# Optimization experiments

Measured on AMD Instinct MI355X. Metric: run time of the kernel, lower is better.

Reference implementation:

```python
import jax, jax.numpy as jnp
import numpy as np

DEPTH, DIM, HEADS, DH, MLP, N, B = 6, 192, 12, 16, 768, 256, 32
INNER = HEADS * DH  # 192


def setup_inputs() -> dict:
    key = jax.random.key(0)
    ks = jax.random.split(key, 10)
    w = lambda i, shape: jax.random.normal(ks[i], shape, dtype=jnp.float32) * 0.02
    return {
        'x': jax.random.normal(ks[0], (B, N, DIM), dtype=jnp.float32),
        'ln1_g': jnp.ones((DEPTH, DIM), jnp.float32),
        'ln1_b': jnp.zeros((DEPTH, DIM), jnp.float32),
        'Wq': w(1, (DEPTH, DIM, INNER)),
        'Wkv': w(2, (DEPTH, DIM, 2 * INNER)),
        'lsa_scale': jnp.full((DEPTH, HEADS), DH ** -0.5, dtype=jnp.float32),
        'mix_pre': jax.random.normal(ks[3], (DEPTH, HEADS, HEADS), dtype=jnp.float32),
        'mix_post': jax.random.normal(ks[4], (DEPTH, HEADS, HEADS), dtype=jnp.float32),
        'Wo': w(5, (DEPTH, INNER, DIM)),
        'bo': jnp.zeros((DEPTH, DIM), jnp.float32),
        'ls1': jnp.full((DEPTH, DIM), 0.1, dtype=jnp.float32),
        'ln2_g': jnp.ones((DEPTH, DIM), jnp.float32),
        'ln2_b': jnp.zeros((DEPTH, DIM), jnp.float32),
        'W1': w(6, (DEPTH, DIM, MLP)),
        'b1': jnp.zeros((DEPTH, MLP), jnp.float32),
        'W2': w(7, (DEPTH, MLP, DIM)),
        'b2': jnp.zeros((DEPTH, DIM), jnp.float32),
        'ls2': jnp.full((DEPTH, DIM), 0.1, dtype=jnp.float32),
    }


def _ln(x, g, b, eps=1e-5):
    m = x.mean(-1, keepdims=True)
    v = ((x - m) ** 2).mean(-1, keepdims=True)
    return (x - m) * jax.lax.rsqrt(v + eps) * g + b


def _heads(t, b, n):
    # (b, n, h*d) -> (b, h, n, d)
    return t.reshape(b, n, HEADS, DH).transpose(0, 2, 1, 3)


def _forward(x, ln1_g, ln1_b, Wq, Wkv, lsa_scale, mix_pre, mix_post, Wo, bo,
             ls1, ln2_g, ln2_b, W1, b1, W2, b2, ls2):
    b, n, _ = x.shape
    diag = jnp.arange(n)
    for l in range(DEPTH):
        # --- PreNorm + talking-heads LSA attention + LayerScale(0.1) ---
        h = _ln(x, ln1_g[l], ln1_b[l])
        q = _heads(h @ Wq[l], b, n)
        k, v = jnp.split(h @ Wkv[l], 2, axis=-1)
        k, v = _heads(k, b, n), _heads(v, b, n)
        dots = jnp.einsum('bhid,bhjd->bhij', q, k) * lsa_scale[l][None, :, None, None]
        # LSA: source sets diagonal to -1e-09 (literal, near-zero) when if_patch_attn
        dots = dots.at[:, :, diag, diag].set(-1e-9)
        dots = jnp.einsum('bhij,hg->bgij', dots, mix_pre[l])
        a = jax.nn.softmax(dots, axis=-1)
        a = jnp.einsum('bhij,hg->bgij', a, mix_post[l])
        o = jnp.einsum('bhij,bhjd->bhid', a, v)
        o = o.transpose(0, 2, 1, 3).reshape(b, n, INNER) @ Wo[l] + bo[l]
        x = x + o * ls1[l]
        # --- PreNorm + GELU FFN + LayerScale(0.1) ---
        h2 = _ln(x, ln2_g[l], ln2_b[l])
        f = jax.nn.gelu(h2 @ W1[l] + b1[l], approximate=False) @ W2[l] + b2[l]
        x = x + f * ls2[l]
    return x


def reference(x, ln1_g, ln1_b, Wq, Wkv, lsa_scale, mix_pre, mix_post, Wo, bo,
              ls1, ln2_g, ln2_b, W1, b1, W2, b2, ls2):
    return _forward(x, ln1_g, ln1_b, Wq, Wkv, lsa_scale, mix_pre, mix_post, Wo,
                    bo, ls1, ln2_g, ln2_b, W1, b1, W2, b2, ls2)
```

## Files before the change

kernel.cpp:

```cpp
#include <hip/hip_runtime.h>
#include <hip/hip_bf16.h>

#define DEPTH   6
#define DIM     192
#define HEADS   12
#define DH      16
#define MLPD    768
#define SEQ     256
#define BATCH   32
#define ROWS    (BATCH*SEQ)

typedef __attribute__((ext_vector_type(8))) short short8;
typedef __attribute__((ext_vector_type(4))) float f32x4;
typedef __attribute__((ext_vector_type(4))) _Float16 half4;
typedef __attribute__((ext_vector_type(8))) _Float16 half8;
typedef __hip_bfloat16 bf16_t;
typedef _Float16 f16_t;

__device__ __forceinline__ bf16_t f2b(float v){ return __float2bfloat16(v); }
__device__ __forceinline__ ushort f2u(float v){
    union{ bf16_t b; ushort u; } w; w.b = __float2bfloat16(v); return w.u;
}
__device__ __forceinline__ f16_t u2h(ushort u){ union{ ushort u; f16_t h; } w; w.u = u; return w.h; }
__device__ __forceinline__ ushort h2u(f16_t h){ union{ ushort u; f16_t h; } w; w.h = h; return w.u; }

__device__ __forceinline__ void async16(ushort* lds, const ushort* gp){
    __builtin_amdgcn_global_load_lds(
        (const __attribute__((address_space(1))) uint*)gp,
        (__attribute__((address_space(3))) uint*)lds, 16, 0, 0);
}

__global__ void copy_kernel(const float* __restrict__ x, float* __restrict__ xr, int n){
    int i = blockIdx.x*256 + threadIdx.x;
    if (i < n) xr[i] = x[i];
}

__device__ __forceinline__ void wt_tile(const float* __restrict__ W,
        ushort* __restrict__ WT, int K, int N, int l, int tx, int ty,
        int tid, ushort* T){
    const float* src = W + ((size_t)l*K + tx*64)*N + ty*64;
    ushort* dst = WT + ((size_t)l*N + ty*64)*K + tx*64;
    int r = tid >> 2, c4 = (tid & 3)*16;
    #pragma unroll
    for (int u=0; u<4; u++){
        float4 v = *(const float4*)(src + (size_t)r*N + c4 + u*4);
        T[(c4+u*4+0)*72 + r] = f2u(v.x);
        T[(c4+u*4+1)*72 + r] = f2u(v.y);
        T[(c4+u*4+2)*72 + r] = f2u(v.z);
        T[(c4+u*4+3)*72 + r] = f2u(v.w);
    }
    __syncthreads();
    int n = tid >> 2, k8 = (tid & 3)*16;
    #pragma unroll
    for (int u=0; u<2; u++)
        *(uint4*)(dst + (size_t)n*K + k8 + u*8) = *(uint4*)&T[n*72 + k8 + u*8];
}

__global__ __launch_bounds__(256) void wt_all(
        const float* __restrict__ Wq, const float* __restrict__ Wkv,
        const float* __restrict__ Wo, const float* __restrict__ W1,
        const float* __restrict__ W2,
        ushort* __restrict__ WqT, ushort* __restrict__ WkvT,
        ushort* __restrict__ WoT, ushort* __restrict__ W1T,
        ushort* __restrict__ W2T){
    __shared__ ushort T[64*72];
    int id = blockIdx.x, l = blockIdx.y, tid = threadIdx.x;
    if (id < 9)       wt_tile(Wq,  WqT,  192, 192, l, id/3,       id%3,       tid, T);
    else if (id < 27) wt_tile(Wkv, WkvT, 192, 384, l, (id-9)/6,   (id-9)%6,   tid, T);
    else if (id < 36) wt_tile(Wo,  WoT,  192, 192, l, (id-27)/3,  (id-27)%3,  tid, T);
    else if (id < 72) wt_tile(W1,  W1T,  192, 768, l, (id-36)/12, (id-36)%12, tid, T);
    else              wt_tile(W2,  W2T,  768, 192, l, (id-72)/3,  (id-72)%3,  tid, T);
}

__global__ __launch_bounds__(256) void ln_kernel(
        const float* __restrict__ xres, const float* __restrict__ ln_g,
        const float* __restrict__ ln_b, ushort* __restrict__ out){
    int lane = threadIdx.x & 63, w = threadIdx.x >> 6;
    int row = blockIdx.x*4 + w;
    const float* xr = xres + (size_t)row*DIM;
    float v0 = xr[lane], v1 = xr[lane+64], v2 = xr[lane+128];
    float s = v0+v1+v2;
    #pragma unroll
    for (int off=32; off; off>>=1) s += __shfl_xor(s, off, 64);
    float m = s*(1.0f/192.0f);
    float d0=v0-m, d1=v1-m, d2=v2-m;
    float q = d0*d0+d1*d1+d2*d2;
    #pragma unroll
    for (int off=32; off; off>>=1) q += __shfl_xor(q, off, 64);
    float inv = rsqrtf(q*(1.0f/192.0f) + 1e-5f);
    float g0 = ln_g[lane], g1 = ln_g[lane+64], g2 = ln_g[lane+128];
    float e0 = ln_b[lane], e1 = ln_b[lane+64], e2 = ln_b[lane+128];
    ushort* dst = out + (size_t)row*DIM;
    dst[lane]     = f2u(d0*inv*g0 + e0);
    dst[lane+64]  = f2u(d1*inv*g1 + e1);
    dst[lane+128] = f2u(d2*inv*g2 + e2);
}

template<int MODE>
__global__ __launch_bounds__(256) void gemm_ln_kernel(
        const ushort* __restrict__ Aln, const ushort* __restrict__ BT0,
        const ushort* __restrict__ BT1, const float* __restrict__ bias,
        f16_t* __restrict__ out0, f16_t* __restrict__ out1,
        f16_t* __restrict__ out2){
    __shared__ ushort As[6*2048];
    __shared__ ushort Bs[6*2048];
    int tid = threadIdx.x, lane = tid & 63, w = tid >> 6;
    int bm = blockIdx.x*64;
    int bn = blockIdx.y*64;
    {
        const ushort* ap = Aln + (size_t)(bm + (tid>>2))*DIM + (tid&3)*8;
        const ushort* bt; int bnl;
        if (MODE == 0 && bn >= DIM){ bt = BT1; bnl = bn - DIM; }
        else { bt = BT0; bnl = bn; }
        const ushort* bp = bt + (size_t)(bnl + (tid>>2))*DIM + (tid&3)*8;
        #pragma unroll
        for (int c=0; c<6; c++){
            async16(&As[c*2048 + tid*8], ap + c*32);
            async16(&Bs[c*2048 + tid*8], bp + c*32);
        }
    }
    __syncthreads();
    int wrow = w >> 1, wcol = w & 1;
    int quad = lane >> 4, mr = lane & 15;
    f32x4 acc[2][2] = {};
    #pragma unroll
    for (int c = 0; c < 6; c++){
        short8 a0 = *(const short8*)&As[c*2048 + (wrow*32+mr)*32    + quad*8];
        short8 a1 = *(const short8*)&As[c*2048 + (wrow*32+16+mr)*32 + quad*8];
        short8 b0 = *(const short8*)&Bs[c*2048 + (wcol*32+mr)*32    + quad*8];
        short8 b1 = *(const short8*)&Bs[c*2048 + (wcol*32+16+mr)*32 + quad*8];
        acc[0][0] = __builtin_amdgcn_mfma_f32_16x16x32_bf16(a0, b0, acc[0][0], 0,0,0);
        acc[0][1] = __builtin_amdgcn_mfma_f32_16x16x32_bf16(a0, b1, acc[0][1], 0,0,0);
        acc[1][0] = __builtin_amdgcn_mfma_f32_16x16x32_bf16(a1, b0, acc[1][0], 0,0,0);
        acc[1][1] = __builtin_amdgcn_mfma_f32_16x16x32_bf16(a1, b1, acc[1][1], 0,0,0);
    }
    #pragma unroll
    for (int rr=0; rr<2; rr++){
        #pragma unroll
        for (int cc=0; cc<2; cc++){
            int col = bn + wcol*32 + cc*16 + mr;
            if (MODE == 0){
                if (col < 2*DIM){
                    f16_t* op = (col < DIM) ? (out0 + col) : (out1 + col - DIM);
                    #pragma unroll
                    for (int tt=0; tt<4; tt++){
                        int row = bm + wrow*32 + rr*16 + quad*4 + tt;
                        op[(size_t)row*DIM] = (f16_t)acc[rr][cc][tt];
                    }
                } else {
                    int d = col - 2*DIM;
                    int row0 = bm + wrow*32 + rr*16 + quad*4;
                    int bb = row0 >> 8, j0 = row0 & 255;
                    half4 pk;
                    #pragma unroll
                    for (int tt=0; tt<4; tt++) pk[tt] = (f16_t)acc[rr][cc][tt];
                    *(half4*)(out2 + (((size_t)(bb*DIM + d)) << 8) + j0) = pk;
                }
            } else {
                float bv = bias[col];
                #pragma unroll
                for (int tt=0; tt<4; tt++){
                    int row = bm + wrow*32 + rr*16 + quad*4 + tt;
                    float z = acc[rr][cc][tt] + bv;
                    ((bf16_t*)out0)[(size_t)row*MLPD + col] =
                        f2b(0.5f*z*(1.0f + erff(z*0.70710678118654752f)));
                }
            }
        }
    }
}

template<int ROUNDS>
__global__ __launch_bounds__(256) void gemm_a_kernel(
        const ushort* __restrict__ A, const ushort* __restrict__ BT,
        const float* __restrict__ bias, const float* __restrict__ ls,
        float* __restrict__ xres){
    const int K = ROUNDS*192;
    __shared__ ushort As[6*2048];
    __shared__ ushort Bs[6*2048];
    int tid = threadIdx.x, lane = tid & 63, w = tid >> 6;
    int wrow = w >> 1, wcol = w & 1;
    int bm = blockIdx.x*64, bn = blockIdx.y*64;
    int quad = lane >> 4, mr = lane & 15;
    const ushort* ap = A  + (size_t)(bm + (tid>>2))*K + (tid&3)*8;
    const ushort* bp = BT + (size_t)(bn + (tid>>2))*K + (tid&3)*8;
    f32x4 acc[2][2] = {};
    for (int r = 0; r < ROUNDS; r++){
        #pragma unroll
        for (int c=0; c<6; c++){
            async16(&As[c*2048 + tid*8], ap + r*192 + c*32);
            async16(&Bs[c*2048 + tid*8], bp + r*192 + c*32);
        }
        __syncthreads();
        #pragma unroll
        for (int c=0; c<6; c++){
            short8 a0 = *(const short8*)&As[c*2048 + (wrow*32+mr)*32    + quad*8];
            short8 a1 = *(const short8*)&As[c*2048 + (wrow*32+16+mr)*32 + quad*8];
            short8 b0 = *(const short8*)&Bs[c*2048 + (wcol*32+mr)*32    + quad*8];
            short8 b1 = *(const short8*)&Bs[c*2048 + (wcol*32+16+mr)*32 + quad*8];
            acc[0][0] = __builtin_amdgcn_mfma_f32_16x16x32_bf16(a0, b0, acc[0][0], 0,0,0);
            acc[0][1] = __builtin_amdgcn_mfma_f32_16x16x32_bf16(a0, b1, acc[0][1], 0,0,0);
            acc[1][0] = __builtin_amdgcn_mfma_f32_16x16x32_bf16(a1, b0, acc[1][0], 0,0,0);
            acc[1][1] = __builtin_amdgcn_mfma_f32_16x16x32_bf16(a1, b1, acc[1][1], 0,0,0);
        }
        if (r+1 < ROUNDS) __syncthreads();
    }
    #pragma unroll
    for (int rr=0; rr<2; rr++){
        #pragma unroll
        for (int cc=0; cc<2; cc++){
            int col = bn + wcol*32 + cc*16 + mr;
            float bv = bias[col], lv = ls[col];
            #pragma unroll
            for (int tt=0; tt<4; tt++){
                int row = bm + wrow*32 + rr*16 + quad*4 + tt;
                xres[(size_t)row*DIM + col] += (acc[rr][cc][tt] + bv)*lv;
            }
        }
    }
}

#define SLAB     4488
#define IST      280
#define ROWP     200
#define Q_OFF    53856
#define POST_OFF 57056
#define PRE_OFF  57312
#define X_OFF    57456
#define LTOT     63856

__global__ __launch_bounds__(1024, 1) void attn_kernel(
        const f16_t* __restrict__ qb, const f16_t* __restrict__ kb,
        const f16_t* __restrict__ vTg,
        const float* __restrict__ lsa, const float* __restrict__ pre,
        const float* __restrict__ post, const ushort* __restrict__ WoT,
        const float* __restrict__ bo, const float* __restrict__ ls1,
        const float* __restrict__ ln2g, const float* __restrict__ ln2b,
        ushort* __restrict__ lnb, float* __restrict__ xres){
    __shared__ ushort L[LTOT];
    int tid  = threadIdx.x;
    int lane = tid & 63, w = tid >> 6;
    int quad = lane >> 4, nr = lane & 15;
    int b  = blockIdx.x >> 4;
    int i0 = (blockIdx.x & 15) << 4;

    if (tid < 384){
        int e = tid*8, i = e/DIM, d = e%DIM, hh = d >> 4;
        float sc = lsa[hh];
        union { uint4 v; f16_t h[8]; } iv, ov;
        iv.v = *(const uint4*)(qb + (size_t)(b*SEQ + i0 + i)*DIM + d);
        #pragma unroll
        for (int u=0; u<8; u++) ov.h[u] = (f16_t)((float)iv.h[u]*sc);
        *(uint4*)&L[Q_OFF + i*ROWP + d] = ov.v;
    } else if (tid < 512){
        for (int k = tid-384; k < 256; k += 128){
            int gg = k >> 4, hh = k & 15;
            L[POST_OFF + k] = (gg < 12 && hh < 12) ? h2u((f16_t)post[hh*12+gg])
                                                   : (ushort)0;
        }
    } else if (tid < 640){
        for (int k = tid-512; k < 144; k += 128)
            L[PRE_OFF + k] = h2u((f16_t)pre[k]);
    }
    __syncthreads();

    half4 postTf = *(const half4*)&L[POST_OFF + nr*16 + quad*4];

    {
        int jg = w*16 + nr;
        const f16_t* krow = kb + (size_t)(b*SEQ + jg)*DIM;
        half8 qh[6], kh[6];
        #pragma unroll
        for (int c=0; c<6; c++){
            union{ short8 s; half8 h; } a, k2;
            a.s  = *(const short8*)&L[Q_OFF + nr*ROWP + c*32 + quad*8];
            k2.s = *(const short8*)(const void*)(krow + c*32 + quad*8);
            qh[c] = a.h; kh[c] = k2.h;
        }
        int dd = jg - (i0 + quad*4);
        int hb = (quad>>1)*12;
        #pragma unroll
        for (int g=0; g<12; g++){
            f32x4 a = {0,0,0,0};
            #pragma unroll
            for (int c=0; c<6; c++){
                f16_t s = u2h(L[PRE_OFF + hb + c*24 + g]);
                a = __builtin_amdgcn_mfma_f32_16x16x32_f16(qh[c]*s, kh[c], a, 0,0,0);
            }
            ushort* sp = &L[g*SLAB + jg];
            sp[(quad*4+0)*IST] = (dd==0) ? (ushort)0 : h2u((f16_t)a[0]);
            sp[(quad*4+1)*IST] = (dd==1) ? (ushort)0 : h2u((f16_t)a[1]);
            sp[(quad*4+2)*IST] = (dd==2) ? (ushort)0 : h2u((f16_t)a[2]);
            sp[(quad*4+3)*IST] = (dd==3) ? (ushort)0 : h2u((f16_t)a[3]);
        }
    }
    __syncthreads();

    for (int r = w; r < 192; r += 16){
        int g = r >> 4, i = r & 15;
        ushort* sp = &L[g*SLAB + i*IST];
        ushort4 uv = *(ushort4*)&sp[lane*4];
        float e0 = __expf((float)u2h(uv.x));
        float e1 = __expf((float)u2h(uv.y));
        float e2 = __expf((float)u2h(uv.z));
        float e3 = __expf((float)u2h(uv.w));
        float ssum = e0+e1+e2+e3;
        #pragma unroll
        for (int off=32; off; off>>=1) ssum += __shfl_xor(ssum, off, 64);
        float rin = 1.0f/ssum;
        uv.x = h2u((f16_t)(e0*rin)); uv.y = h2u((f16_t)(e1*rin));
        uv.z = h2u((f16_t)(e2*rin)); uv.w = h2u((f16_t)(e3*rin));
        *(ushort4*)&sp[lane*4] = uv;
    }
    __syncthreads();

    for (int s = 0; s < 16; s++){
        int cb = s*16 + w;
        int i = cb >> 4, jb = cb & 15;
        int colbase = i*IST + jb*16 + nr;
        half4 bv;
        #pragma unroll
        for (int t=0; t<4; t++){
            int hs = quad*4 + t; if (hs > 11) hs = 11;
            bv[t] = u2h(L[hs*SLAB + colbase]);
        }
        f32x4 cc = __builtin_amdgcn_mfma_f32_16x16x16f16(postTf, bv, (f32x4){0,0,0,0}, 0,0,0);
        if (quad < 3){
            #pragma unroll
            for (int t=0; t<4; t++) L[(quad*4+t)*SLAB + colbase] = h2u((f16_t)cc[t]);
        }
    }
    __syncthreads();

    f32x4 oacc = {0,0,0,0};
    if (w < 12){
        int g = w;
        const f16_t* vrow = vTg + (((size_t)(b*DIM + g*16 + nr)) << 8);
        #pragma unroll
        for (int c = 0; c < 4; c++){
            #pragma unroll
            for (int ks = 0; ks < 4; ks++){
                int jl = c*64 + ks*16 + quad*4;
                half4 av = *(const half4*)&L[g*SLAB + nr*IST + jl];
                half4 bv = *(const half4*)(vrow + jl);
                oacc = __builtin_amdgcn_mfma_f32_16x16x16f16(av, bv, oacc, 0,0,0);
            }
        }
    }

    if (w < 12){
        int g = w;
        #pragma unroll
        for (int t=0; t<4; t++){
            int i = quad*4 + t;
            L[Q_OFF + i*ROWP + g*16 + nr] = f2u(oacc[t]);
        }
    }
    __syncthreads();

    float* X = (float*)&L[X_OFF];
    if (w < 12){
        f32x4 wacc = {0,0,0,0};
        int ct = w;
        const ushort* wg = WoT + (size_t)(ct*16 + nr)*192;
        #pragma unroll
        for (int c = 0; c < 3; c++){
            #pragma unroll
            for (int sub = 0; sub < 2; sub++){
                int k0 = c*64 + sub*32;
                short8 av = *(const short8*)&L[Q_OFF + nr*ROWP + k0 + quad*8];
                short8 bv = *(const short8*)(wg + k0 + quad*8);
                wacc = __builtin_amdgcn_mfma_f32_16x16x32_bf16(av, bv, wacc, 0,0,0);
            }
        }
        int col = ct*16 + nr;
        float bv2 = bo[col], lv = ls1[col];
        #pragma unroll
        for (int t=0; t<4; t++){
            int i = quad*4 + t;
            int row = b*SEQ + i0 + i;
            float upd = xres[(size_t)row*DIM + col] + (wacc[t] + bv2)*lv;
            xres[(size_t)row*DIM + col] = upd;
            X[i*200 + col] = upd;
        }
    }
    __syncthreads();

    {
        int i = w;
        float v0 = X[i*200 + lane], v1 = X[i*200 + lane+64], v2 = X[i*200 + lane+128];
        float s = v0+v1+v2;
        #pragma unroll
        for (int off=32; off; off>>=1) s += __shfl_xor(s, off, 64);
        float m = s*(1.0f/192.0f);
        float d0=v0-m, d1=v1-m, d2=v2-m;
        float q = d0*d0+d1*d1+d2*d2;
        #pragma unroll
        for (int off=32; off; off>>=1) q += __shfl_xor(q, off, 64);
        float inv = rsqrtf(q*(1.0f/192.0f) + 1e-5f);
        float g0 = ln2g[lane], g1 = ln2g[lane+64], g2 = ln2g[lane+128];
        float e0 = ln2b[lane], e1 = ln2b[lane+64], e2 = ln2b[lane+128];
        ushort* dst = lnb + (size_t)(b*SEQ + i0 + i)*DIM;
        dst[lane]     = f2u(d0*inv*g0 + e0);
        dst[lane+64]  = f2u(d1*inv*g1 + e1);
        dst[lane+128] = f2u(d2*inv*g2 + e2);
    }
}

extern "C" void kernel_launch(void* const* d_in, const int* in_sizes, int n_in,
                              void* d_out, int out_size, void* d_ws, size_t ws_size,
                              hipStream_t stream){
    const float* x    = (const float*)d_in[0];
    const float* ln1g = (const float*)d_in[1];
    const float* ln1b = (const float*)d_in[2];
    const float* Wq   = (const float*)d_in[3];
    const float* Wkv  = (const float*)d_in[4];
    const float* lsa  = (const float*)d_in[5];
    const float* pre  = (const float*)d_in[6];
    const float* post = (const float*)d_in[7];
    const float* Wo   = (const float*)d_in[8];
    const float* bo   = (const float*)d_in[9];
    const float* ls1  = (const float*)d_in[10];
    const float* ln2g = (const float*)d_in[11];
    const float* ln2b = (const float*)d_in[12];
    const float* W1   = (const float*)d_in[13];
    const float* b1   = (const float*)d_in[14];
    const float* W2   = (const float*)d_in[15];
    const float* b2   = (const float*)d_in[16];
    const float* ls2  = (const float*)d_in[17];
    float* xres = (float*)d_out;

    char* ws = (char*)d_ws;
    f16_t*  qb  = (f16_t*)ws;
    f16_t*  kb  = (f16_t*)(ws + (size_t)ROWS*DIM*2);
    f16_t*  vT  = (f16_t*)(ws + (size_t)ROWS*DIM*4);
    bf16_t* fb  = (bf16_t*)ws;
    char* p = ws + (size_t)ROWS*MLPD*2;
    ushort* WqT  = (ushort*)p; p += (size_t)DEPTH*DIM*DIM*2;
    ushort* WkvT = (ushort*)p; p += (size_t)DEPTH*DIM*2*DIM*2;
    ushort* WoT  = (ushort*)p; p += (size_t)DEPTH*DIM*DIM*2;
    ushort* W1T  = (ushort*)p; p += (size_t)DEPTH*DIM*MLPD*2;
    ushort* W2T  = (ushort*)p; p += (size_t)DEPTH*MLPD*DIM*2;
    ushort* lnb  = (ushort*)p; p += (size_t)ROWS*DIM*2;

    int ntot = ROWS*DIM;
    copy_kernel<<<ntot/256, 256, 0, stream>>>(x, xres, ntot);
    wt_all<<<dim3(108, 6), 256, 0, stream>>>(Wq, Wkv, Wo, W1, W2,
                                             WqT, WkvT, WoT, W1T, W2T);
    for (int l = 0; l < DEPTH; l++){
        ln_kernel<<<ROWS/4, 256, 0, stream>>>(xres, ln1g + l*DIM, ln1b + l*DIM, lnb);
        gemm_ln_kernel<0><<<dim3(128,9), 256, 0, stream>>>(lnb,
                WqT + (size_t)l*DIM*DIM, WkvT + (size_t)l*DIM*2*DIM,
                nullptr, qb, kb, vT);
        attn_kernel<<<BATCH*(SEQ/16), 1024, 0, stream>>>(qb, kb, vT,
                lsa + l*HEADS, pre + l*HEADS*HEADS, post + l*HEADS*HEADS,
                WoT + (size_t)l*DIM*DIM, bo + l*DIM, ls1 + l*DIM,
                ln2g + l*DIM, ln2b + l*DIM, lnb, xres);
        gemm_ln_kernel<1><<<dim3(128,12), 256, 0, stream>>>(lnb,
                W1T + (size_t)l*DIM*MLPD, nullptr, b1 + l*MLPD, (f16_t*)fb, nullptr,
                nullptr);
        gemm_a_kernel<4><<<dim3(128,3), 256, 0, stream>>>((const ushort*)fb,
                W2T + (size_t)l*MLPD*DIM, b2 + l*DIM, ls2 + l*DIM, xres);
    }
}
```

Baseline: 620.0 us.

## Restructure attention kernel to per-head warps with register-resident scores

The attention kernel now uses 12 waves, one per mixed head, instead of 16 waves. Each wave computes its full 16x256 score tile in registers and does the softmax there with a cross-lane reduction. The post-mix and PV product run in two halves of 128 keys each, so shared memory drops from about 128KB to about 58KB and launch bounds allow several blocks per CU. This aims to raise occupancy and cut LDS round trips, at the cost of more register pressure, redundant K loads per wave, and extra barriers between the halves.

```diff
diff --git a/kernel.cpp b/kernel.cpp
--- a/kernel.cpp
+++ b/kernel.cpp
@@ -220,16 +220,15 @@
     }
 }
 
-#define SLAB     4488
-#define IST      280
+#define HP       2120
+#define IP       132
+#define Q_OFF    25440
 #define ROWP     200
-#define Q_OFF    53856
-#define POST_OFF 57056
-#define PRE_OFF  57312
-#define X_OFF    57456
-#define LTOT     63856
-
-__global__ __launch_bounds__(1024, 1) void attn_kernel(
+#define POST_OFF 28640
+#define PRE_OFF  28896
+#define LTOT     29040
+
+__global__ __launch_bounds__(768, 6) void attn_kernel(
         const f16_t* __restrict__ qb, const f16_t* __restrict__ kb,
         const f16_t* __restrict__ vTg,
         const float* __restrict__ lsa, const float* __restrict__ pre,
@@ -241,8 +240,9 @@
     int tid  = threadIdx.x;
     int lane = tid & 63, w = tid >> 6;
     int quad = lane >> 4, nr = lane & 15;
-    int b  = blockIdx.x >> 4;
-    int i0 = (blockIdx.x & 15) << 4;
+    int b   = blockIdx.x >> 4;
+    int it0 = blockIdx.x & 15;
+    int i0  = it0 << 4;
 
     if (tid < 384){
         int e = tid*8, i = e/DIM, d = e%DIM, hh = d >> 4;
@@ -265,104 +265,106 @@
     __syncthreads();
 
     half4 postTf = *(const half4*)&L[POST_OFF + nr*16 + quad*4];
-
+    const int g = w;
+
+    const f16_t* kbase = kb + (size_t)b*SEQ*DIM;
+    half4 ph4[16];
+    #pragma unroll
+    for (int pass=0; pass<2; pass++){
+        f32x4 acc[8];
+        #pragma unroll
+        for (int jl=0; jl<8; jl++) acc[jl] = (f32x4){0,0,0,0};
+        #pragma unroll
+        for (int c=0; c<6; c++){
+            union{ short8 s; half8 h; } a;
+            a.s = *(const short8*)&L[Q_OFF + nr*ROWP + c*32 + quad*8];
+            f16_t sc = u2h(L[PRE_OFF + (quad>>1)*12 + c*24 + g]);
+            half8 qf = a.h * sc;
+            #pragma unroll
+            for (int jl=0; jl<8; jl++){
+                int jt = pass*8 + jl;
+                union{ short8 s; half8 h; } kf;
+                kf.s = *(const short8*)(const void*)
+                        (kbase + (size_t)(jt*16 + nr)*DIM + c*32 + quad*8);
+                acc[jl] = __builtin_amdgcn_mfma_f32_16x16x32_f16(kf.h, qf, acc[jl], 0,0,0);
+            }
+        }
+        #pragma unroll
+        for (int jl=0; jl<8; jl++){
+            int jt = pass*8 + jl;
+            #pragma unroll
+            for (int t=0; t<4; t++){
+                bool dg = (jt == it0) && (quad*4 + t == nr);
+                ph4[jt][t] = dg ? (f16_t)0.0f : (f16_t)acc[jl][t];
+            }
+        }
+    }
+
+    float rs = 0.f;
+    #pragma unroll
+    for (int jt=0; jt<16; jt++)
+        #pragma unroll
+        for (int t=0; t<4; t++) rs += __expf((float)ph4[jt][t]);
+    rs += __shfl_xor(rs, 16, 64);
+    rs += __shfl_xor(rs, 32, 64);
+    float rin = 1.0f/rs;
+
+    f32x4 oacc = {0,0,0,0};
+    #pragma unroll
+    for (int hf=0; hf<2; hf++){
+        #pragma unroll
+        for (int jl=0; jl<8; jl++){
+            int jt = hf*8 + jl;
+            half4 pw;
+            #pragma unroll
+            for (int t=0; t<4; t++)
+                pw[t] = (f16_t)(__expf((float)ph4[jt][t]) * rin);
+            *(half4*)&L[g*HP + nr*IP + jl*16 + quad*4] = pw;
+        }
+        __syncthreads();
+        for (int s=0; s<11; s++){
+            int cb = s*12 + w;
+            if (cb < 128){
+                int i = cb >> 3, jc = cb & 7;
+                int colb = i*IP + jc*16 + nr;
+                half4 bv;
+                #pragma unroll
+                for (int t=0; t<4; t++){
+                    int hs = quad*4 + t; if (hs > 11) hs = 11;
+                    bv[t] = u2h(L[hs*HP + colb]);
+                }
+                f32x4 cc = __builtin_amdgcn_mfma_f32_16x16x16f16(postTf, bv,
+                                                (f32x4){0,0,0,0}, 0,0,0);
+                if (quad < 3){
+                    #pragma unroll
+                    for (int t=0; t<4; t++)
+                        L[(quad*4+t)*HP + colb] = h2u((f16_t)cc[t]);
+                }
+            }
+        }
+        __syncthreads();
+        const f16_t* vrow = vTg + (((size_t)(b*DIM + g*16 + nr)) << 8) + hf*128;
+        #pragma unroll
+        for (int ks=0; ks<8; ks++){
+            int jl = ks*16 + quad*4;
+            half4 av  = *(const half4*)&L[g*HP + nr*IP + jl];
+            half4 bvv = *(const half4*)(vrow + jl);
+            oacc = __builtin_amdgcn_mfma_f32_16x16x16f16(av, bvv, oacc, 0,0,0);
+        }
+        if (hf == 0) __syncthreads();
+    }
+
+    #pragma unroll
+    for (int t=0; t<4; t++){
+        int i = quad*4 + t;
+        L[Q_OFF + i*ROWP + g*16 + nr] = f2u(oacc[t]);
+    }
+    __syncthreads();
+
+    float* X = (float*)&L[0];
     {
-        int jg = w*16 + nr;
-        const f16_t* krow = kb + (size_t)(b*SEQ + jg)*DIM;
-        half8 qh[6], kh[6];
-        #pragma unroll
-        for (int c=0; c<6; c++){
-            union{ short8 s; half8 h; } a, k2;
-            a.s  = *(const short8*)&L[Q_OFF + nr*ROWP + c*32 + quad*8];
-            k2.s = *(const short8*)(const void*)(krow + c*32 + quad*8);
-            qh[c] = a.h; kh[c] = k2.h;
-        }
-        int dd = jg - (i0 + quad*4);
-        int hb = (quad>>1)*12;
-        #pragma unroll
-        for (int g=0; g<12; g++){
-            f32x4 a = {0,0,0,0};
-            #pragma unroll
-            for (int c=0; c<6; c++){
-                f16_t s = u2h(L[PRE_OFF + hb + c*24 + g]);
-                a = __builtin_amdgcn_mfma_f32_16x16x32_f16(qh[c]*s, kh[c], a, 0,0,0);
-            }
-            ushort* sp = &L[g*SLAB + jg];
-            sp[(quad*4+0)*IST] = (dd==0) ? (ushort)0 : h2u((f16_t)a[0]);
-            sp[(quad*4+1)*IST] = (dd==1) ? (ushort)0 : h2u((f16_t)a[1]);
-            sp[(quad*4+2)*IST] = (dd==2) ? (ushort)0 : h2u((f16_t)a[2]);
-            sp[(quad*4+3)*IST] = (dd==3) ? (ushort)0 : h2u((f16_t)a[3]);
-        }
-    }
-    __syncthreads();
-
-    for (int r = w; r < 192; r += 16){
-        int g = r >> 4, i = r & 15;
-        ushort* sp = &L[g*SLAB + i*IST];
-        ushort4 uv = *(ushort4*)&sp[lane*4];
-        float e0 = __expf((float)u2h(uv.x));
-        float e1 = __expf((float)u2h(uv.y));
-        float e2 = __expf((float)u2h(uv.z));
-        float e3 = __expf((float)u2h(uv.w));
-        float ssum = e0+e1+e2+e3;
-        #pragma unroll
-        for (int off=32; off; off>>=1) ssum += __shfl_xor(ssum, off, 64);
-        float rin = 1.0f/ssum;
-        uv.x = h2u((f16_t)(e0*rin)); uv.y = h2u((f16_t)(e1*rin));
-        uv.z = h2u((f16_t)(e2*rin)); uv.w = h2u((f16_t)(e3*rin));
-        *(ushort4*)&sp[lane*4] = uv;
-    }
-    __syncthreads();
-
-    for (int s = 0; s < 16; s++){
-        int cb = s*16 + w;
-        int i = cb >> 4, jb = cb & 15;
-        int colbase = i*IST + jb*16 + nr;
-        half4 bv;
-        #pragma unroll
-        for (int t=0; t<4; t++){
-            int hs = quad*4 + t; if (hs > 11) hs = 11;
-            bv[t] = u2h(L[hs*SLAB + colbase]);
-        }
-        f32x4 cc = __builtin_amdgcn_mfma_f32_16x16x16f16(postTf, bv, (f32x4){0,0,0,0}, 0,0,0);
-        if (quad < 3){
-            #pragma unroll
-            for (int t=0; t<4; t++) L[(quad*4+t)*SLAB + colbase] = h2u((f16_t)cc[t]);
-        }
-    }
-    __syncthreads();
-
-    f32x4 oacc = {0,0,0,0};
-    if (w < 12){
-        int g = w;
-        const f16_t* vrow = vTg + (((size_t)(b*DIM + g*16 + nr)) << 8);
-        #pragma unroll
-        for (int c = 0; c < 4; c++){
-            #pragma unroll
-            for (int ks = 0; ks < 4; ks++){
-                int jl = c*64 + ks*16 + quad*4;
-                half4 av = *(const half4*)&L[g*SLAB + nr*IST + jl];
-                half4 bv = *(const half4*)(vrow + jl);
-                oacc = __builtin_amdgcn_mfma_f32_16x16x16f16(av, bv, oacc, 0,0,0);
-            }
-        }
-    }
-
-    if (w < 12){
-        int g = w;
-        #pragma unroll
-        for (int t=0; t<4; t++){
-            int i = quad*4 + t;
-            L[Q_OFF + i*ROWP + g*16 + nr] = f2u(oacc[t]);
-        }
-    }
-    __syncthreads();
-
-    float* X = (float*)&L[X_OFF];
-    if (w < 12){
         f32x4 wacc = {0,0,0,0};
-        int ct = w;
-        const ushort* wg = WoT + (size_t)(ct*16 + nr)*192;
+        const ushort* wg = WoT + (size_t)(g*16 + nr)*192;
         #pragma unroll
         for (int c = 0; c < 3; c++){
             #pragma unroll
@@ -373,7 +375,7 @@
                 wacc = __builtin_amdgcn_mfma_f32_16x16x32_bf16(av, bv, wacc, 0,0,0);
             }
         }
-        int col = ct*16 + nr;
+        int col = g*16 + nr;
         float bv2 = bo[col], lv = ls1[col];
         #pragma unroll
         for (int t=0; t<4; t++){
@@ -386,8 +388,7 @@
     }
     __syncthreads();
 
-    {
-        int i = w;
+    for (int i = w; i < 16; i += 12){
         float v0 = X[i*200 + lane], v1 = X[i*200 + lane+64], v2 = X[i*200 + lane+128];
         float s = v0+v1+v2;
         #pragma unroll
@@ -452,7 +453,7 @@
         gemm_ln_kernel<0><<<dim3(128,9), 256, 0, stream>>>(lnb,
                 WqT + (size_t)l*DIM*DIM, WkvT + (size_t)l*DIM*2*DIM,
                 nullptr, qb, kb, vT);
-        attn_kernel<<<BATCH*(SEQ/16), 1024, 0, stream>>>(qb, kb, vT,
+        attn_kernel<<<BATCH*(SEQ/16), 768, 0, stream>>>(qb, kb, vT,
                 lsa + l*HEADS, pre + l*HEADS*HEADS, post + l*HEADS*HEADS,
                 WoT + (size_t)l*DIM*DIM, bo + l*DIM, ls1 + l*DIM,
                 ln2g + l*DIM, ln2b + l*DIM, lnb, xres);
```

Measured after the change: 1.193 ms. 1.92x slower.
